# Optimization experiments

Measured on AMD Instinct MI355X. Metric: run time of the kernel, lower is better.

Reference implementation:

```python
import jax, jax.numpy as jnp
import numpy as np

BS, K, VOCAB = 128, 8, 50257

def setup_inputs() -> dict:
    key = jax.random.key(0)
    k1, k2, k3, k4 = jax.random.split(key, 4)
    logits = jax.random.normal(k1, (BS * K + BS, VOCAB), dtype=jnp.float32)
    temperatures = jax.random.uniform(k2, (BS,), minval=0.5, maxval=1.5, dtype=jnp.float32)
    draft_token_ids = jax.random.randint(k3, (BS, K), 0, VOCAB)
    dlogits = jax.random.normal(k4, (BS * K, VOCAB), dtype=jnp.float32)
    draft_probs = jax.nn.softmax(dlogits, axis=-1)  # valid draft distribution per row
    return {"draft_token_ids": draft_token_ids, "logits": logits,
            "temperatures": temperatures, "draft_probs": draft_probs}

def reference(draft_token_ids, logits, temperatures, draft_probs):
    bs, k = draft_token_ids.shape
    vocab = logits.shape[-1]
    n_draft = bs * k
    nkey = jax.random.key(42)
    ku, kg_rec, kg_bonus = jax.random.split(nkey, 3)

    # --- bonus token sampling (inner `sampler`): categorical over softmax(logits/temp)
    # via the Gumbel-max trick (equivalent to torch.multinomial on the softmax probs)
    bonus_logits = logits[n_draft:] / temperatures[:, None]            # [bs, vocab]
    g_bonus = jax.random.gumbel(kg_bonus, (bs, vocab), dtype=jnp.float32)
    bonus_ids = jnp.argmax(bonus_logits + g_bonus, axis=-1)           # [bs]

    # --- target probabilities for draft positions
    target_logits = logits[:n_draft].reshape(bs, k, vocab) / temperatures[:, None, None]
    target_probs = jax.nn.softmax(target_logits, axis=-1)              # [bs,k,vocab]
    dprobs = draft_probs.reshape(bs, k, vocab)

    # per-position probs of the proposed draft token
    p_t = jnp.take_along_axis(target_probs, draft_token_ids[..., None], axis=-1)[..., 0]
    p_d = jnp.take_along_axis(dprobs, draft_token_ids[..., None], axis=-1)[..., 0]
    accept_prob = jnp.where(p_d > 0.0,
                            jnp.minimum(1.0, p_t / jnp.maximum(p_d, 1e-30)),
                            0.0)                                       # [bs,k]
    u = jax.random.uniform(ku, (bs, k), dtype=jnp.float32)
    accept = u <= accept_prob                                          # [bs,k]

    # accepted prefix length: number of leading accepts
    prefix = jnp.cumprod(accept.astype(jnp.int32), axis=1)
    n_acc = prefix.sum(axis=1)                                         # [bs] in [0,k]

    # --- recovery sampling: multinomial over clamp(target - draft, 0), renormalized;
    # fall back to target_probs if residual mass is zero. Gumbel-max on log weights
    # is invariant to normalization, so no explicit division by the mass is needed.
    rec = jnp.maximum(target_probs - dprobs, 0.0)                      # [bs,k,vocab]
    mass = rec.sum(axis=-1, keepdims=True)
    rec_dist = jnp.where(mass > 0.0, rec, target_probs)
    g_rec = jax.random.gumbel(kg_rec, (bs, k, vocab), dtype=jnp.float32)
    recovered = jnp.argmax(jnp.log(jnp.maximum(rec_dist, 1e-30)) + g_rec, axis=-1)  # [bs,k]

    # recovered token at the first rejected position (clipped gather; masked below)
    rej_pos = jnp.minimum(n_acc, k - 1)
    rec_at = jnp.take_along_axis(recovered, rej_pos[:, None], axis=1)[:, 0]  # [bs]

    # --- assemble padded output [bs, k+1]: accepted draft prefix, then either
    # recovered token (if a rejection occurred) or bonus token (all accepted); -1 pad.
    pos = jnp.arange(k + 1)[None, :]
    draft_pad = jnp.concatenate(
        [draft_token_ids, jnp.zeros((bs, 1), dtype=draft_token_ids.dtype)], axis=1)
    final_tok = jnp.where(n_acc[:, None] == k, bonus_ids[:, None], rec_at[:, None])
    out = jnp.where(pos < n_acc[:, None], draft_pad,
                    jnp.where(pos == n_acc[:, None], final_tok, -1))
    return out
```

## Files before the change

### kernel.cpp

```cpp
#include <hip/hip_runtime.h>
#include <cstdint>

#define VOCAB  50257
#define BSZ    128
#define KD     8
#define NDRAFT (BSZ * KD)
#define SEG    16
#define SEGLEN 3142

__host__ __device__ inline uint32_t rotl32(uint32_t x, int r) {
  return (x << r) | (x >> (32 - r));
}

__host__ __device__ inline void threefry2x32(uint32_t k0, uint32_t k1,
                                             uint32_t x0, uint32_t x1,
                                             uint32_t& o0, uint32_t& o1) {
  uint32_t ks2 = k0 ^ k1 ^ 0x1BD11BDAu;
  x0 += k0; x1 += k1;
  x0 += x1; x1 = rotl32(x1, 13); x1 ^= x0;
  x0 += x1; x1 = rotl32(x1, 15); x1 ^= x0;
  x0 += x1; x1 = rotl32(x1, 26); x1 ^= x0;
  x0 += x1; x1 = rotl32(x1,  6); x1 ^= x0;
  x0 += k1; x1 += ks2 + 1u;
  x0 += x1; x1 = rotl32(x1, 17); x1 ^= x0;
  x0 += x1; x1 = rotl32(x1, 29); x1 ^= x0;
  x0 += x1; x1 = rotl32(x1, 16); x1 ^= x0;
  x0 += x1; x1 = rotl32(x1, 24); x1 ^= x0;
  x0 += ks2; x1 += k0 + 2u;
  x0 += x1; x1 = rotl32(x1, 13); x1 ^= x0;
  x0 += x1; x1 = rotl32(x1, 15); x1 ^= x0;
  x0 += x1; x1 = rotl32(x1, 26); x1 ^= x0;
  x0 += x1; x1 = rotl32(x1,  6); x1 ^= x0;
  x0 += k0; x1 += k1 + 3u;
  x0 += x1; x1 = rotl32(x1, 17); x1 ^= x0;
  x0 += x1; x1 = rotl32(x1, 29); x1 ^= x0;
  x0 += x1; x1 = rotl32(x1, 16); x1 ^= x0;
  x0 += x1; x1 = rotl32(x1, 24); x1 ^= x0;
  x0 += k1; x1 += ks2 + 4u;
  x0 += x1; x1 = rotl32(x1, 13); x1 ^= x0;
  x0 += x1; x1 = rotl32(x1, 15); x1 ^= x0;
  x0 += x1; x1 = rotl32(x1, 26); x1 ^= x0;
  x0 += x1; x1 = rotl32(x1,  6); x1 ^= x0;
  x0 += ks2; x1 += k0 + 5u;
  o0 = x0; o1 = x1;
}

__device__ inline uint32_t tf_bits32(uint32_t k0, uint32_t k1, uint64_t idx) {
  uint32_t o0, o1;
  threefry2x32(k0, k1, (uint32_t)(idx >> 32), (uint32_t)idx, o0, o1);
  return o0 ^ o1;
}

__device__ inline float bits_to_f01(uint32_t bits) {
  return __uint_as_float((bits >> 9) | 0x3f800000u) - 1.0f;
}

__device__ inline float gumbel_fast(uint32_t bits) {
  const float tiny = 1.1754943508222875e-38f;
  float u = fmaxf(tiny, bits_to_f01(bits) + tiny);
  return -__logf(-__logf(u));
}

__device__ inline unsigned long long pack_si(float s, int idx) {
  uint32_t u = __float_as_uint(s);
  u = (u & 0x80000000u) ? ~u : (u | 0x80000000u);
  return ((unsigned long long)u << 32) | (uint32_t)(VOCAB - idx);
}
__device__ inline int unpack_idx(unsigned long long p) {
  return VOCAB - (int)(p & 0xFFFFFFFFu);
}

__global__ __launch_bounds__(256) void k_stats_bonus(
    const float* __restrict__ logits, const float* __restrict__ temps,
    float* __restrict__ row_max, float* __restrict__ row_sum,
    unsigned long long* __restrict__ bon_pack,
    uint32_t kb0, uint32_t kb1) {
  int tid = threadIdx.x;
  if ((int)blockIdx.x < NDRAFT) {
    int row = blockIdx.x;
    float inv_t = 1.0f / temps[row >> 3];
    const float* x = logits + (size_t)row * VOCAB;
    float m_t = -INFINITY, s_t = 0.0f;
    auto upd = [&](float val) {
      float xs = val * inv_t;
      float nm = fmaxf(m_t, xs);
      s_t = s_t * __expf(m_t - nm) + __expf(xs - nm);
      m_t = nm;
    };
    int pre = (4 - (row & 3)) & 3;
    if (tid < pre) upd(x[tid]);
    int nv = (VOCAB - pre) >> 2;
    const float4* xv = (const float4*)(x + pre);
    for (int i = tid; i < nv; i += 256) {
      float4 q = xv[i];
      upd(q.x); upd(q.y); upd(q.z); upd(q.w);
    }
    for (int v = pre + 4 * nv + tid; v < VOCAB; v += 256) upd(x[v]);

    __shared__ float sm[256], ss[256];
    sm[tid] = m_t; ss[tid] = s_t;
    __syncthreads();
    for (int st = 128; st > 0; st >>= 1) {
      if (tid < st) {
        float m2 = sm[tid + st], s2 = ss[tid + st];
        float M = fmaxf(sm[tid], m2);
        ss[tid] = ss[tid] * __expf(sm[tid] - M) + s2 * __expf(m2 - M);
        sm[tid] = M;
      }
      __syncthreads();
    }
    if (tid == 0) { row_max[row] = sm[0]; row_sum[row] = ss[0]; }
  } else {
    int r = blockIdx.x - NDRAFT;
    int b = r >> 4, seg = r & 15;
    int v0 = seg * SEGLEN;
    int v1 = v0 + SEGLEN; if (v1 > VOCAB) v1 = VOCAB;
    float inv_t = 1.0f / temps[b];
    const float* x = logits + (size_t)(NDRAFT + b) * VOCAB;
    uint64_t base = (uint64_t)b * VOCAB;
    float bv = -INFINITY; int bi = VOCAB;
    for (int v = v0 + tid; v < v1; v += 256) {
      float sc = x[v] * inv_t + gumbel_fast(tf_bits32(kb0, kb1, base + v));
      if (sc > bv) { bv = sc; bi = v; }
    }
    __shared__ unsigned long long sp[256];
    sp[tid] = pack_si(bv, bi);
    __syncthreads();
    for (int st = 128; st > 0; st >>= 1) {
      if (tid < st) { if (sp[tid + st] > sp[tid]) sp[tid] = sp[tid + st]; }
      __syncthreads();
    }
    if (tid == 0) atomicMax(&bon_pack[b], sp[0]);
  }
}

__global__ void k_accept(const int* __restrict__ dtok,
                         const float* __restrict__ logits,
                         const float* __restrict__ temps,
                         const float* __restrict__ dprobs,
                         const float* __restrict__ row_max,
                         const float* __restrict__ row_sum,
                         int* __restrict__ n_acc,
                         uint32_t ku0, uint32_t ku1) {
  __shared__ int acc_flags[NDRAFT];
  int i = threadIdx.x;
  {
    int b = i >> 3;
    int tok = dtok[i];
    float t  = temps[b];
    float xt = logits[(size_t)i * VOCAB + tok] / t;
    float pt = expf(xt - row_max[i]) / row_sum[i];
    float pd = dprobs[(size_t)i * VOCAB + tok];
    float ap = (pd > 0.0f) ? fminf(1.0f, pt / fmaxf(pd, 1e-30f)) : 0.0f;
    float u  = bits_to_f01(tf_bits32(ku0, ku1, (uint64_t)i));
    acc_flags[i] = (u <= ap) ? 1 : 0;
  }
  __syncthreads();
  if (i < BSZ) {
    int n = 0;
    for (int j = 0; j < KD; j++) {
      if (acc_flags[i * KD + j]) n++;
      else break;
    }
    n_acc[i] = n;
  }
}

__global__ __launch_bounds__(256) void k_recover(
    const float* __restrict__ logits, const float* __restrict__ temps,
    const float* __restrict__ dprobs,
    const float* __restrict__ row_max, const float* __restrict__ row_sum,
    const int* __restrict__ n_acc,
    unsigned long long* __restrict__ rec_pc,
    unsigned long long* __restrict__ rec_pp,
    int* __restrict__ rec_any,
    uint32_t kr0, uint32_t kr1) {
  int r = blockIdx.x;
  int b = r >> 4, seg = r & 15;
  int n = n_acc[b];
  if (n >= KD) return;
  int tid = threadIdx.x;
  int row = b * KD + n;
  int v0 = seg * SEGLEN;
  int v1 = v0 + SEGLEN; if (v1 > VOCAB) v1 = VOCAB;
  float inv_t = 1.0f / temps[b];
  float m = row_max[row];
  float inv_s = 1.0f / row_sum[row];
  const float* x  = logits + (size_t)row * VOCAB;
  const float* pd = dprobs + (size_t)row * VOCAB;
  uint64_t base = (uint64_t)row * VOCAB;

  float bc = -INFINITY, bp = -INFINITY;
  int ic = VOCAB, ip = VOCAB, any = 0;
  for (int v = v0 + tid; v < v1; v += 256) {
    float pt = __expf(x[v] * inv_t - m) * inv_s;
    float diff = pt - pd[v];
    if (diff > 0.0f) any = 1;
    float g = gumbel_fast(tf_bits32(kr0, kr1, base + v));
    float scc = __logf(fmaxf(fmaxf(diff, 0.0f), 1e-30f)) + g;
    float scp = __logf(fmaxf(pt, 1e-30f)) + g;
    if (scc > bc) { bc = scc; ic = v; }
    if (scp > bp) { bp = scp; ip = v; }
  }
  __shared__ unsigned long long sp[256];
  __shared__ int sa[256];
  sp[tid] = pack_si(bc, ic); sa[tid] = any;
  __syncthreads();
  for (int st = 128; st > 0; st >>= 1) {
    if (tid < st) {
      if (sp[tid + st] > sp[tid]) sp[tid] = sp[tid + st];
      sa[tid] |= sa[tid + st];
    }
    __syncthreads();
  }
  if (tid == 0) {
    atomicMax(&rec_pc[b], sp[0]);
    if (sa[0]) atomicOr(&rec_any[b], 1);
  }
  __syncthreads();
  sp[tid] = pack_si(bp, ip);
  __syncthreads();
  for (int st = 128; st > 0; st >>= 1) {
    if (tid < st) { if (sp[tid + st] > sp[tid]) sp[tid] = sp[tid + st]; }
    __syncthreads();
  }
  if (tid == 0) atomicMax(&rec_pp[b], sp[0]);
}

__global__ void k_final(const int* __restrict__ dtok,
                        const int* __restrict__ n_acc,
                        const unsigned long long* __restrict__ bon_pack,
                        const unsigned long long* __restrict__ rec_pc,
                        const unsigned long long* __restrict__ rec_pp,
                        const int* __restrict__ rec_any,
                        int* __restrict__ out) {
  int idx = blockIdx.x * blockDim.x + threadIdx.x;
  if (idx >= BSZ * (KD + 1)) return;
  int b = idx / (KD + 1), p = idx % (KD + 1);
  int n = n_acc[b];
  int val;
  if (p < n)       val = dtok[b * KD + p];
  else if (p == n) {
    if (n == KD) val = unpack_idx(bon_pack[b]);
    else         val = unpack_idx(rec_any[b] ? rec_pc[b] : rec_pp[b]);
  }
  else             val = -1;
  out[idx] = val;
}

extern "C" void kernel_launch(void* const* d_in, const int* in_sizes, int n_in,
                              void* d_out, int out_size, void* d_ws, size_t ws_size,
                              hipStream_t stream) {
  const int*   dtok   = (const int*)  d_in[0];
  const float* logits = (const float*)d_in[1];
  const float* temps  = (const float*)d_in[2];
  const float* dprobs = (const float*)d_in[3];
  int* out = (int*)d_out;

  unsigned long long* bon_pack = (unsigned long long*)d_ws;
  unsigned long long* rec_pc   = bon_pack + BSZ;
  unsigned long long* rec_pp   = rec_pc + BSZ;
  int*   rec_any = (int*)(rec_pp + BSZ);
  float* row_max = (float*)(rec_any + BSZ);
  float* row_sum = row_max + NDRAFT;
  int*   n_acc   = (int*)(row_sum + NDRAFT);

  uint32_t ku0, ku1, kr0, kr1, kb0, kb1;
  threefry2x32(0u, 42u, 0u, 0u, ku0, ku1);
  threefry2x32(0u, 42u, 0u, 1u, kr0, kr1);
  threefry2x32(0u, 42u, 0u, 2u, kb0, kb1);

  hipMemsetAsync(d_ws, 0, (size_t)(3 * BSZ * 8 + BSZ * 4), stream);

  k_stats_bonus<<<NDRAFT + BSZ * SEG, 256, 0, stream>>>(
      logits, temps, row_max, row_sum, bon_pack, kb0, kb1);
  k_accept<<<1, NDRAFT, 0, stream>>>(dtok, logits, temps, dprobs,
                                     row_max, row_sum, n_acc, ku0, ku1);
  k_recover<<<BSZ * SEG, 256, 0, stream>>>(logits, temps, dprobs,
                                           row_max, row_sum, n_acc,
                                           rec_pc, rec_pp, rec_any, kr0, kr1);
  k_final<<<(BSZ * (KD + 1) + 255) / 256, 256, 0, stream>>>(
      dtok, n_acc, bon_pack, rec_pc, rec_pp, rec_any, out);
}
```

Measured before the change: 440.8 us.

## Fuse accept test into stats kernel and vectorize recover loads with nontemporal hints

Removes the single-block k_accept launch. Each stats block now evaluates the accept test for its own row and sets a bit in a per-batch bitmask through atomicOr. The accepted-prefix length is derived with a count-trailing-zeros on that mask. The stats loop is unrolled by two float4 loads and now uses nontemporal loads. The recover kernel reads logits and draft probs as float4 nontemporal loads over an aligned segment split, with head and tail handled separately. This trims a serial launch and some load overhead, at the cost of extra atomics and more complex indexing.

Measured after the change: 425.7 us. 3.4% less time.

```diff
diff --git a/kernel.cpp b/kernel.cpp
--- a/kernel.cpp
+++ b/kernel.cpp
@@ -7,6 +7,12 @@
 #define NDRAFT (BSZ * KD)
 #define SEG    16
 #define SEGLEN 3142
+
+typedef float fx4 __attribute__((ext_vector_type(4)));
+
+__device__ inline fx4 ntload4(const fx4* p) {
+  return __builtin_nontemporal_load(p);
+}
 
 __host__ __device__ inline uint32_t rotl32(uint32_t x, int r) {
   return (x << r) | (x >> (32 - r));
@@ -70,16 +76,32 @@
   return VOCAB - (int)(p & 0xFFFFFFFFu);
 }
 
+__device__ inline int nacc_from_bits(int bits) {
+  return __builtin_ctz(~bits & 0x1FF);
+}
+
 __global__ __launch_bounds__(256) void k_stats_bonus(
     const float* __restrict__ logits, const float* __restrict__ temps,
+    const int* __restrict__ dtok, const float* __restrict__ dprobs,
     float* __restrict__ row_max, float* __restrict__ row_sum,
+    int* __restrict__ acc_bits,
     unsigned long long* __restrict__ bon_pack,
-    uint32_t kb0, uint32_t kb1) {
+    uint32_t kb0, uint32_t kb1, uint32_t ku0, uint32_t ku1) {
   int tid = threadIdx.x;
   if ((int)blockIdx.x < NDRAFT) {
     int row = blockIdx.x;
-    float inv_t = 1.0f / temps[row >> 3];
+    int b = row >> 3;
+    float t = temps[b];
+    float inv_t = 1.0f / t;
     const float* x = logits + (size_t)row * VOCAB;
+
+    int tok = 0; float x_tok = 0.0f, pd_tok = 0.0f;
+    if (tid == 0) {
+      tok    = dtok[row];
+      x_tok  = x[tok];
+      pd_tok = dprobs[(size_t)row * VOCAB + tok];
+    }
+
     float m_t = -INFINITY, s_t = 0.0f;
     auto upd = [&](float val) {
       float xs = val * inv_t;
@@ -90,9 +112,16 @@
     int pre = (4 - (row & 3)) & 3;
     if (tid < pre) upd(x[tid]);
     int nv = (VOCAB - pre) >> 2;
-    const float4* xv = (const float4*)(x + pre);
-    for (int i = tid; i < nv; i += 256) {
-      float4 q = xv[i];
+    const fx4* xv = (const fx4*)(x + pre);
+    int i = tid;
+    for (; i + 256 < nv; i += 512) {
+      fx4 q0 = ntload4(xv + i);
+      fx4 q1 = ntload4(xv + i + 256);
+      upd(q0.x); upd(q0.y); upd(q0.z); upd(q0.w);
+      upd(q1.x); upd(q1.y); upd(q1.z); upd(q1.w);
+    }
+    for (; i < nv; i += 256) {
+      fx4 q = ntload4(xv + i);
       upd(q.x); upd(q.y); upd(q.z); upd(q.w);
     }
     for (int v = pre + 4 * nv + tid; v < VOCAB; v += 256) upd(x[v]);
@@ -109,7 +138,15 @@
       }
       __syncthreads();
     }
-    if (tid == 0) { row_max[row] = sm[0]; row_sum[row] = ss[0]; }
+    if (tid == 0) {
+      float M = sm[0], S = ss[0];
+      row_max[row] = M; row_sum[row] = S;
+      float xt = x_tok / t;
+      float pt = expf(xt - M) / S;
+      float ap = (pd_tok > 0.0f) ? fminf(1.0f, pt / fmaxf(pd_tok, 1e-30f)) : 0.0f;
+      float u  = bits_to_f01(tf_bits32(ku0, ku1, (uint64_t)row));
+      if (u <= ap) atomicOr(&acc_bits[b], 1 << (row & 7));
+    }
   } else {
     int r = blockIdx.x - NDRAFT;
     int b = r >> 4, seg = r & 15;
@@ -134,55 +171,21 @@
   }
 }
 
-__global__ void k_accept(const int* __restrict__ dtok,
-                         const float* __restrict__ logits,
-                         const float* __restrict__ temps,
-                         const float* __restrict__ dprobs,
-                         const float* __restrict__ row_max,
-                         const float* __restrict__ row_sum,
-                         int* __restrict__ n_acc,
-                         uint32_t ku0, uint32_t ku1) {
-  __shared__ int acc_flags[NDRAFT];
-  int i = threadIdx.x;
-  {
-    int b = i >> 3;
-    int tok = dtok[i];
-    float t  = temps[b];
-    float xt = logits[(size_t)i * VOCAB + tok] / t;
-    float pt = expf(xt - row_max[i]) / row_sum[i];
-    float pd = dprobs[(size_t)i * VOCAB + tok];
-    float ap = (pd > 0.0f) ? fminf(1.0f, pt / fmaxf(pd, 1e-30f)) : 0.0f;
-    float u  = bits_to_f01(tf_bits32(ku0, ku1, (uint64_t)i));
-    acc_flags[i] = (u <= ap) ? 1 : 0;
-  }
-  __syncthreads();
-  if (i < BSZ) {
-    int n = 0;
-    for (int j = 0; j < KD; j++) {
-      if (acc_flags[i * KD + j]) n++;
-      else break;
-    }
-    n_acc[i] = n;
-  }
-}
-
 __global__ __launch_bounds__(256) void k_recover(
     const float* __restrict__ logits, const float* __restrict__ temps,
     const float* __restrict__ dprobs,
     const float* __restrict__ row_max, const float* __restrict__ row_sum,
-    const int* __restrict__ n_acc,
+    const int* __restrict__ acc_bits,
     unsigned long long* __restrict__ rec_pc,
     unsigned long long* __restrict__ rec_pp,
     int* __restrict__ rec_any,
     uint32_t kr0, uint32_t kr1) {
   int r = blockIdx.x;
   int b = r >> 4, seg = r & 15;
-  int n = n_acc[b];
+  int n = nacc_from_bits(acc_bits[b]);
   if (n >= KD) return;
   int tid = threadIdx.x;
   int row = b * KD + n;
-  int v0 = seg * SEGLEN;
-  int v1 = v0 + SEGLEN; if (v1 > VOCAB) v1 = VOCAB;
   float inv_t = 1.0f / temps[b];
   float m = row_max[row];
   float inv_s = 1.0f / row_sum[row];
@@ -192,16 +195,41 @@
 
   float bc = -INFINITY, bp = -INFINITY;
   int ic = VOCAB, ip = VOCAB, any = 0;
-  for (int v = v0 + tid; v < v1; v += 256) {
-    float pt = __expf(x[v] * inv_t - m) * inv_s;
-    float diff = pt - pd[v];
+
+  auto proc = [&](float xval, float pdval, int v) {
+    float pt = __expf(xval * inv_t - m) * inv_s;
+    float diff = pt - pdval;
     if (diff > 0.0f) any = 1;
-    float g = gumbel_fast(tf_bits32(kr0, kr1, base + v));
+    float g = gumbel_fast(tf_bits32(kr0, kr1, base + (uint64_t)v));
     float scc = __logf(fmaxf(fmaxf(diff, 0.0f), 1e-30f)) + g;
     float scp = __logf(fmaxf(pt, 1e-30f)) + g;
     if (scc > bc) { bc = scc; ic = v; }
     if (scp > bp) { bp = scp; ip = v; }
-  }
+  };
+
+  int pre = (4 - (row & 3)) & 3;
+  int nv = (VOCAB - pre) >> 2;
+  const fx4* xv = (const fx4*)(x + pre);
+  const fx4* pv = (const fx4*)(pd + pre);
+  int per = (nv + SEG - 1) / SEG;
+  int s0 = seg * per;
+  int s1 = s0 + per; if (s1 > nv) s1 = nv;
+  for (int i = s0 + tid; i < s1; i += 256) {
+    fx4 qx = ntload4(xv + i);
+    fx4 qp = ntload4(pv + i);
+    int v = pre + 4 * i;
+    proc(qx.x, qp.x, v);
+    proc(qx.y, qp.y, v + 1);
+    proc(qx.z, qp.z, v + 2);
+    proc(qx.w, qp.w, v + 3);
+  }
+  if (seg == 0) {
+    if (tid < pre) proc(x[tid], pd[tid], tid);
+  }
+  if (seg == SEG - 1) {
+    for (int v = pre + 4 * nv + tid; v < VOCAB; v += 256) proc(x[v], pd[v], v);
+  }
+
   __shared__ unsigned long long sp[256];
   __shared__ int sa[256];
   sp[tid] = pack_si(bc, ic); sa[tid] = any;
@@ -228,7 +256,7 @@
 }
 
 __global__ void k_final(const int* __restrict__ dtok,
-                        const int* __restrict__ n_acc,
+                        const int* __restrict__ acc_bits,
                         const unsigned long long* __restrict__ bon_pack,
                         const unsigned long long* __restrict__ rec_pc,
                         const unsigned long long* __restrict__ rec_pp,
@@ -237,7 +265,7 @@
   int idx = blockIdx.x * blockDim.x + threadIdx.x;
   if (idx >= BSZ * (KD + 1)) return;
   int b = idx / (KD + 1), p = idx % (KD + 1);
-  int n = n_acc[b];
+  int n = nacc_from_bits(acc_bits[b]);
   int val;
   if (p < n)       val = dtok[b * KD + p];
   else if (p == n) {
@@ -260,25 +288,24 @@
   unsigned long long* bon_pack = (unsigned long long*)d_ws;
   unsigned long long* rec_pc   = bon_pack + BSZ;
   unsigned long long* rec_pp   = rec_pc + BSZ;
-  int*   rec_any = (int*)(rec_pp + BSZ);
-  float* row_max = (float*)(rec_any + BSZ);
-  float* row_sum = row_max + NDRAFT;
-  int*   n_acc   = (int*)(row_sum + NDRAFT);
+  int*   rec_any  = (int*)(rec_pp + BSZ);
+  int*   acc_bits = rec_any + BSZ;
+  float* row_max  = (float*)(acc_bits + BSZ);
+  float* row_sum  = row_max + NDRAFT;
 
   uint32_t ku0, ku1, kr0, kr1, kb0, kb1;
   threefry2x32(0u, 42u, 0u, 0u, ku0, ku1);
   threefry2x32(0u, 42u, 0u, 1u, kr0, kr1);
   threefry2x32(0u, 42u, 0u, 2u, kb0, kb1);
 
-  hipMemsetAsync(d_ws, 0, (size_t)(3 * BSZ * 8 + BSZ * 4), stream);
+  hipMemsetAsync(d_ws, 0, (size_t)(3 * BSZ * 8 + 2 * BSZ * 4), stream);
 
   k_stats_bonus<<<NDRAFT + BSZ * SEG, 256, 0, stream>>>(
-      logits, temps, row_max, row_sum, bon_pack, kb0, kb1);
-  k_accept<<<1, NDRAFT, 0, stream>>>(dtok, logits, temps, dprobs,
-                                     row_max, row_sum, n_acc, ku0, ku1);
+      logits, temps, dtok, dprobs, row_max, row_sum, acc_bits, bon_pack,
+      kb0, kb1, ku0, ku1);
   k_recover<<<BSZ * SEG, 256, 0, stream>>>(logits, temps, dprobs,
-                                           row_max, row_sum, n_acc,
+                                           row_max, row_sum, acc_bits,
                                            rec_pc, rec_pp, rec_any, kr0, kr1);
   k_final<<<(BSZ * (KD + 1) + 255) / 256, 256, 0, stream>>>(
-      dtok, n_acc, bon_pack, rec_pc, rec_pp, rec_any, out);
-}
+      dtok, acc_bits, bon_pack, rec_pc, rec_pp, rec_any, out);
+}
```
